# Kernel optimization log

Measured on AMD Instinct MI355X. Metric: run time of the kernel, lower is better.

The kernel has to match this reference:

```python
import jax, jax.numpy as jnp
import numpy as np
from jax import lax

EPS = 1e-5

@jax.custom_vjp
def binarize(x):
    return jnp.sign(x)

def _bin_fwd(x):
    return jnp.sign(x), x

def _bin_bwd(x, g):
    # straight-through estimator: pass grad where |x| <= 1
    return (g * (jnp.abs(x) <= 1.0).astype(g.dtype),)

binarize.defvjp(_bin_fwd, _bin_bwd)


def bconv(x, w, stride=1, pad=0):
    # BinarizeConv2d: sign-binarize both activations and weights, dense conv
    return lax.conv_general_dilated(
        binarize(x), binarize(w),
        window_strides=(stride, stride),
        padding=[(pad, pad), (pad, pad)],
        dimension_numbers=('NCHW', 'OIHW', 'NCHW'))


def bn(x, gamma, beta):
    # training-mode batch norm (grad enabled in torch forward): batch stats over (N,H,W)
    mean = x.mean(axis=(0, 2, 3), keepdims=True)
    var = ((x - mean) ** 2).mean(axis=(0, 2, 3), keepdims=True)
    return gamma * (x - mean) * lax.rsqrt(var + EPS) + beta


def hardtanh(x):
    return jnp.clip(x, -1.0, 1.0)


def setup_inputs() -> dict:
    key = jax.random.key(0)
    ks = jax.random.split(key, 4)
    N, Cin, H, W = 64, 256, 56, 56
    P = 64  # planes; expansion*planes == Cin -> identity shortcut
    return {
        'x':  jax.random.normal(ks[0], (N, Cin, H, W), dtype=jnp.float32),
        'w1': jax.random.normal(ks[1], (P, Cin, 1, 1), dtype=jnp.float32),
        'w2': jax.random.normal(ks[2], (P, P, 3, 3), dtype=jnp.float32),
        'w3': jax.random.normal(ks[3], (Cin, P, 1, 1), dtype=jnp.float32),
        'g1': jnp.ones((1, P, 1, 1), jnp.float32),
        'b1': jnp.zeros((1, P, 1, 1), jnp.float32),
        'g2': jnp.ones((1, P, 1, 1), jnp.float32),
        'b2': jnp.zeros((1, P, 1, 1), jnp.float32),
        'g3': jnp.ones((1, Cin, 1, 1), jnp.float32),
        'b3': jnp.zeros((1, Cin, 1, 1), jnp.float32),
    }


def reference(x, w1, w2, w3, g1, b1, g2, b2, g3, b3):
    out = hardtanh(bn(bconv(x, w1), g1, b1))                 # 1x1 binconv + BN + hardtanh
    out = hardtanh(bn(bconv(out, w2, stride=1, pad=1), g2, b2))  # 3x3 binconv + BN + hardtanh
    out = bn(bconv(out, w3), g3, b3)                          # 1x1 binconv + BN
    out = out + x                                             # identity shortcut
    return hardtanh(out)
```

## Files before the change

kernel.cpp:

```cpp
#include <hip/hip_runtime.h>
#include <stdint.h>
#include <math.h>

typedef unsigned long long u64;
typedef long long ll;

#define H_    56
#define W_    56
#define HW_   3136
#define N_    64
#define C_    256
#define P_    64
#define NPIX_ 200704
#define BN_EPS 1e-5

__global__ __launch_bounds__(256) void pack_weights_k(
    const float* __restrict__ w1, const float* __restrict__ w2,
    const float* __restrict__ w3,
    u64* __restrict__ ws1, u64* __restrict__ wn1,
    u64* __restrict__ ws2, u64* __restrict__ wn2, int* __restrict__ b2,
    u64* __restrict__ ws3, u64* __restrict__ wn3, int* __restrict__ b3) {
  int t = blockIdx.x * 256 + threadIdx.x;
  if (t < 64) {
    int co = t;
    for (int ch = 0; ch < 4; ++ch) {
      u64 s = 0, n = 0;
      for (int j = 0; j < 64; ++j) {
        float v = w1[co * 256 + ch * 64 + j];
        s |= ((u64)(v < 0.f)) << j;
        n |= ((u64)(v != 0.f)) << j;
      }
      ws1[co * 4 + ch] = s; wn1[co * 4 + ch] = n;
    }
  } else if (t < 64 + 576) {
    int idx = t - 64, co = idx / 9, tap = idx % 9;
    u64 s = 0, n = 0;
    for (int ci = 0; ci < 64; ++ci) {
      float v = w2[(co * 64 + ci) * 9 + tap];
      s |= ((u64)(v < 0.f)) << ci;
      n |= ((u64)(v != 0.f)) << ci;
    }
    ws2[idx] = s; wn2[idx] = n; b2[idx] = __popcll(n);
  } else if (t < 64 + 576 + 256) {
    int co = t - 640;
    u64 s = 0, n = 0;
    for (int ci = 0; ci < 64; ++ci) {
      float v = w3[co * 64 + ci];
      s |= ((u64)(v < 0.f)) << ci;
      n |= ((u64)(v != 0.f)) << ci;
    }
    ws3[co] = s; wn3[co] = n; b3[co] = __popcll(n);
  }
}

__device__ inline void bn_thresh(u64 S_, u64 Q_, float g, float b,
                                 int* A, int* X) {
  double S = (double)(ll)S_, Q = (double)(ll)Q_;
  double mean = S / (double)NPIX_;
  double var  = Q / (double)NPIX_ - mean * mean;
  double sc   = (double)g / sqrt(var + BN_EPS);
  double sh   = (double)b - mean * sc;
  if (sc > 0.0) {
    double t = -sh / sc;
    t = fmin(fmax(t, -1.0e8), 1.0e8);
    *A = (int)ceil(t); *X = 0;
  } else if (sc < 0.0) {
    double t = -sh / sc;
    t = fmin(fmax(t, -1.0e8), 1.0e8);
    *A = (int)floor(t) + 1; *X = 1;
  } else {
    *A = (int)0x80000000; *X = (sh < 0.0) ? 1 : 0;
  }
}

__global__ __launch_bounds__(256) void pack_x_k(
    const float* __restrict__ x, u64* __restrict__ xs, u64* __restrict__ xn) {
  int t = blockIdx.x * 256 + threadIdx.x;
  int n = t / 1568;
  int pw = (t - n * 1568) * 2;
  const float* xb = x + (size_t)n * (C_ * HW_) + pw;
  size_t p = (size_t)t * 2;
  for (int q = 0; q < 4; ++q) {
    u64 s0 = 0, s1 = 0, n0 = 0, n1 = 0;
    #pragma unroll 16
    for (int j = 0; j < 64; ++j) {
      float2 v = *(const float2*)(xb + (size_t)(q * 64 + j) * HW_);
      u64 bit = 1ull << j;
      if (v.x <  0.f) s0 |= bit;
      if (v.x != 0.f) n0 |= bit;
      if (v.y <  0.f) s1 |= bit;
      if (v.y != 0.f) n1 |= bit;
    }
    ulonglong2 sv; sv.x = s0; sv.y = s1;
    ulonglong2 nv; nv.x = n0; nv.y = n1;
    *(ulonglong2*)(xs + (size_t)q * NPIX_ + p) = sv;
    *(ulonglong2*)(xn + (size_t)q * NPIX_ + p) = nv;
  }
}

template<int MODE>
__global__ __launch_bounds__(256) void conv1_k(
    const u64* __restrict__ xs, const u64* __restrict__ xn,
    const u64* __restrict__ ws1, const u64* __restrict__ wn1,
    u64* __restrict__ gsum, u64* __restrict__ gsq,
    const float* __restrict__ gamma, const float* __restrict__ beta,
    u64* __restrict__ pout) {
  __shared__ ulonglong2 tile[4][256];
  __shared__ int ssum[64], ssq[64];
  int tid = threadIdx.x, co = tid & 63, wv = tid >> 6;
  int base = blockIdx.x * 256;
  #pragma unroll
  for (int q = 0; q < 4; ++q) {
    ulonglong2 v;
    v.x = xs[(size_t)q * NPIX_ + base + tid];
    v.y = xn[(size_t)q * NPIX_ + base + tid];
    tile[q][tid] = v;
  }
  if (MODE == 0 && tid < 64) { ssum[tid] = 0; ssq[tid] = 0; }
  u64 wS[4], wN[4];
  #pragma unroll
  for (int q = 0; q < 4; ++q) { wS[q] = ws1[co * 4 + q]; wN[q] = wn1[co * 4 + q]; }
  int A = 0, X = 0;
  if (MODE == 1) bn_thresh(gsum[co], gsq[co], gamma[co], beta[co], &A, &X);
  __syncthreads();
  int s = 0, qq = 0;
  u64 mw = 0;
  #pragma unroll 2
  for (int i = 0; i < 64; ++i) {
    int px = wv * 64 + i;
    int acc = 0;
    #pragma unroll
    for (int q = 0; q < 4; ++q) {
      ulonglong2 t2 = tile[q][px];
      u64 v = t2.y & wN[q];
      u64 a = ~(t2.x ^ wS[q]) & v;
      acc += 2 * __popcll(a) - __popcll(v);
    }
    if (MODE == 0) { s += acc; qq += acc * acc; }
    else {
      u64 bal = __ballot((acc < A) ^ X);
      mw = (co == i) ? bal : mw;
    }
  }
  if (MODE == 0) {
    atomicAdd(&ssum[co], s); atomicAdd(&ssq[co], qq);
    __syncthreads();
    if (tid < 64) {
      atomicAdd(&gsum[tid], (u64)(ll)ssum[tid]);
      atomicAdd(&gsq[tid],  (u64)(ll)ssq[tid]);
    }
  } else {
    pout[base + wv * 64 + co] = mw;
  }
}

__device__ inline int c2tap(u64 t, u64 ws, u64 wn) {
  return __popcll(~(t ^ ws) & wn);
}

template<int MODE>
__global__ __launch_bounds__(256) void conv2_k(
    const u64* __restrict__ p1,
    const u64* __restrict__ ws2, const u64* __restrict__ wn2,
    u64* __restrict__ gsum, u64* __restrict__ gsq,
    const float* __restrict__ gamma, const float* __restrict__ beta,
    u64* __restrict__ pout) {
  __shared__ u64 tile[6 * W_];
  __shared__ int ssum[64], ssq[64];
  int tid = threadIdx.x, co = tid & 63, wv = tid >> 6;
  int blk = blockIdx.x;
  int n = blk / 14, t0 = blk - n * 14;
  int h0 = t0 * 4;
  const u64* img = p1 + (size_t)n * HW_;
  for (int j = tid; j < 6 * W_; j += 256) {
    int gh = h0 - 1 + j / W_;
    int gw = j - (j / W_) * W_;
    tile[j] = (gh >= 0 && gh < H_) ? img[gh * W_ + gw] : 0ull;
  }
  if (MODE == 0 && tid < 64) { ssum[tid] = 0; ssq[tid] = 0; }
  u64 wS[9], wN[9]; int wB[9], Bs = 0;
  #pragma unroll
  for (int k = 0; k < 9; ++k) {
    wS[k] = ws2[co * 9 + k]; wN[k] = wn2[co * 9 + k];
    wB[k] = __popcll(wN[k]); Bs += wB[k];
  }
  int A = 0, X = 0;
  if (MODE == 1) bn_thresh(gsum[co], gsq[co], gamma[co], beta[co], &A, &X);
  __syncthreads();
  int h = h0 + wv;
  const u64* rA = tile + wv * W_;
  const u64* rB = rA + W_;
  const u64* rC = rB + W_;
  int vA = (h > 0), vC = (h < H_ - 1);
  int s = 0, qq = 0;
  u64 mw = 0;
  if (vA & vC) {
    {
      int P = c2tap(rA[0], wS[1], wN[1]) + c2tap(rA[1], wS[2], wN[2])
            + c2tap(rB[0], wS[4], wN[4]) + c2tap(rB[1], wS[5], wN[5])
            + c2tap(rC[0], wS[7], wN[7]) + c2tap(rC[1], wS[8], wN[8]);
      int acc = 2 * P - (wB[1] + wB[2] + wB[4] + wB[5] + wB[7] + wB[8]);
      if (MODE == 0) { s += acc; qq += acc * acc; }
      else { u64 bal = __ballot((acc < A) ^ X); mw = (co == 0) ? bal : mw; }
    }
    #pragma unroll 2
    for (int w = 1; w < W_ - 1; ++w) {
      int P = c2tap(rA[w-1], wS[0], wN[0]) + c2tap(rA[w], wS[1], wN[1]) + c2tap(rA[w+1], wS[2], wN[2])
            + c2tap(rB[w-1], wS[3], wN[3]) + c2tap(rB[w], wS[4], wN[4]) + c2tap(rB[w+1], wS[5], wN[5])
            + c2tap(rC[w-1], wS[6], wN[6]) + c2tap(rC[w], wS[7], wN[7]) + c2tap(rC[w+1], wS[8], wN[8]);
      int acc = 2 * P - Bs;
      if (MODE == 0) { s += acc; qq += acc * acc; }
      else { u64 bal = __ballot((acc < A) ^ X); mw = (co == w) ? bal : mw; }
    }
    {
      int P = c2tap(rA[W_-2], wS[0], wN[0]) + c2tap(rA[W_-1], wS[1], wN[1])
            + c2tap(rB[W_-2], wS[3], wN[3]) + c2tap(rB[W_-1], wS[4], wN[4])
            + c2tap(rC[W_-2], wS[6], wN[6]) + c2tap(rC[W_-1], wS[7], wN[7]);
      int acc = 2 * P - (wB[0] + wB[1] + wB[3] + wB[4] + wB[6] + wB[7]);
      if (MODE == 0) { s += acc; qq += acc * acc; }
      else { u64 bal = __ballot((acc < A) ^ X); mw = (co == W_ - 1) ? bal : mw; }
    }
  } else {
    for (int w = 0; w < W_; ++w) {
      int wm = w > 0, wp = w < W_ - 1;
      int P = 0, B = 0;
      if (vA) {
        if (wm) { P += c2tap(rA[w-1], wS[0], wN[0]); B += wB[0]; }
        P += c2tap(rA[w], wS[1], wN[1]); B += wB[1];
        if (wp) { P += c2tap(rA[w+1], wS[2], wN[2]); B += wB[2]; }
      }
      if (wm) { P += c2tap(rB[w-1], wS[3], wN[3]); B += wB[3]; }
      P += c2tap(rB[w], wS[4], wN[4]); B += wB[4];
      if (wp) { P += c2tap(rB[w+1], wS[5], wN[5]); B += wB[5]; }
      if (vC) {
        if (wm) { P += c2tap(rC[w-1], wS[6], wN[6]); B += wB[6]; }
        P += c2tap(rC[w], wS[7], wN[7]); B += wB[7];
        if (wp) { P += c2tap(rC[w+1], wS[8], wN[8]); B += wB[8]; }
      }
      int acc = 2 * P - B;
      if (MODE == 0) { s += acc; qq += acc * acc; }
      else { u64 bal = __ballot((acc < A) ^ X); mw = (co == w) ? bal : mw; }
    }
  }
  if (MODE == 0) {
    atomicAdd(&ssum[co], s); atomicAdd(&ssq[co], qq);
    __syncthreads();
    if (tid < 64) {
      atomicAdd(&gsum[tid], (u64)(ll)ssum[tid]);
      atomicAdd(&gsq[tid],  (u64)(ll)ssq[tid]);
    }
  } else {
    if (co < W_) pout[(size_t)n * HW_ + h * W_ + co] = mw;
  }
}

__global__ __launch_bounds__(256) void conv3_stats_k(
    const u64* __restrict__ p2,
    const u64* __restrict__ ws3, const u64* __restrict__ wn3,
    const int* __restrict__ b3,
    u64* __restrict__ gsum, u64* __restrict__ gsq) {
  __shared__ u64 tile[512];
  int t = threadIdx.x;
  int base = blockIdx.x * 512;
  *(ulonglong2*)&tile[t * 2] = *(const ulonglong2*)&p2[base + t * 2];
  u64 s3 = ws3[t], n3 = wn3[t];
  int bb = b3[t];
  __syncthreads();
  int s = 0, q = 0;
  #pragma unroll 4
  for (int i = 0; i < 512; ++i) {
    int yv = 2 * __popcll(~(tile[i] ^ s3) & n3) - bb;
    s += yv; q += yv * yv;
  }
  atomicAdd(&gsum[t], (u64)(ll)s);
  atomicAdd(&gsq[t],  (u64)(ll)q);
}

__global__ __launch_bounds__(256) void final_k(
    const float* __restrict__ x, const u64* __restrict__ p2,
    const u64* __restrict__ ws3, const u64* __restrict__ wn3,
    const int* __restrict__ b3,
    const u64* __restrict__ gsum, const u64* __restrict__ gsq,
    const float* __restrict__ gamma, const float* __restrict__ beta,
    float* __restrict__ out) {
  __shared__ float fsc[2], fsh[2];
  size_t base = (size_t)blockIdx.x * 1024;
  size_t r0 = base / HW_;
  if (threadIdx.x < 2) {
    int c = (int)((r0 + threadIdx.x) % C_);
    double S = (double)(ll)gsum[c], Q = (double)(ll)gsq[c];
    double mean = S / (double)NPIX_;
    double var  = Q / (double)NPIX_ - mean * mean;
    double inv  = 1.0 / sqrt(var + BN_EPS);
    double sc   = (double)gamma[c] * inv;
    fsc[threadIdx.x] = (float)sc;
    fsh[threadIdx.x] = (float)((double)beta[c] - mean * sc);
  }
  __syncthreads();

  size_t idx = base + (size_t)threadIdx.x * 4;
  size_t lin = idx / HW_;
  int rr = (int)(lin - r0);
  int co = (int)(lin % C_);
  int nn = (int)(lin / C_);
  int hw = (int)(idx % HW_);
  int pb = nn * HW_ + hw;
  u64 s3 = ws3[co], n3 = wn3[co];
  int bb = b3[co];
  float sc = fsc[rr], sh = fsh[rr];
  float4 xv = *(const float4*)(x + idx);
  float4 ov;
  int y0 = 2 * __popcll(~(p2[pb + 0] ^ s3) & n3) - bb;
  int y1 = 2 * __popcll(~(p2[pb + 1] ^ s3) & n3) - bb;
  int y2 = 2 * __popcll(~(p2[pb + 2] ^ s3) & n3) - bb;
  int y3 = 2 * __popcll(~(p2[pb + 3] ^ s3) & n3) - bb;
  ov.x = fminf(fmaxf(sc * (float)y0 + sh + xv.x, -1.f), 1.f);
  ov.y = fminf(fmaxf(sc * (float)y1 + sh + xv.y, -1.f), 1.f);
  ov.z = fminf(fmaxf(sc * (float)y2 + sh + xv.z, -1.f), 1.f);
  ov.w = fminf(fmaxf(sc * (float)y3 + sh + xv.w, -1.f), 1.f);
  *(float4*)(out + idx) = ov;
}

extern "C" void kernel_launch(void* const* d_in, const int* in_sizes, int n_in,
                              void* d_out, int out_size, void* d_ws, size_t ws_size,
                              hipStream_t stream) {
  const float* x  = (const float*)d_in[0];
  const float* w1 = (const float*)d_in[1];
  const float* w2 = (const float*)d_in[2];
  const float* w3 = (const float*)d_in[3];
  const float* g1 = (const float*)d_in[4];
  const float* b1 = (const float*)d_in[5];
  const float* g2 = (const float*)d_in[6];
  const float* b2 = (const float*)d_in[7];
  const float* g3 = (const float*)d_in[8];
  const float* b3 = (const float*)d_in[9];
  float* out = (float*)d_out;

  char* base = (char*)d_ws;
  size_t off = 0;
  auto alloc = [&](size_t bytes) -> char* {
    char* p = base + off;
    off = (off + bytes + 255) & ~(size_t)255;
    return p;
  };
  u64* xs   = (u64*)alloc((size_t)NPIX_ * 4 * 8);
  u64* xnz  = (u64*)alloc((size_t)NPIX_ * 4 * 8);
  u64* p1   = (u64*)alloc((size_t)NPIX_ * 8);
  u64* p2   = (u64*)alloc((size_t)NPIX_ * 8);
  u64* ws1  = (u64*)alloc(256 * 8);
  u64* wn1  = (u64*)alloc(256 * 8);
  u64* ws2  = (u64*)alloc(576 * 8);
  u64* wn2  = (u64*)alloc(576 * 8);
  int* bb2  = (int*)alloc(576 * 4);
  u64* ws3  = (u64*)alloc(256 * 8);
  u64* wn3  = (u64*)alloc(256 * 8);
  int* bb3  = (int*)alloc(256 * 4);
  char* stats = alloc(768 * 8);
  u64* sum1 = (u64*)stats;          u64* sq1 = sum1 + 64;
  u64* sum2 = sq1 + 64;             u64* sq2 = sum2 + 64;
  u64* sum3 = sq2 + 64;             u64* sq3 = sum3 + 256;
  (void)ws_size; (void)n_in; (void)in_sizes; (void)out_size;

  hipMemsetAsync(stats, 0, 768 * 8, stream);

  pack_weights_k<<<4, 256, 0, stream>>>(w1, w2, w3, ws1, wn1, ws2, wn2, bb2,
                                        ws3, wn3, bb3);

  pack_x_k<<<392, 256, 0, stream>>>(x, xs, xnz);

  conv1_k<0><<<784, 256, 0, stream>>>(xs, xnz, ws1, wn1, sum1, sq1,
                                      g1, b1, (u64*)nullptr);
  conv1_k<1><<<784, 256, 0, stream>>>(xs, xnz, ws1, wn1, sum1, sq1,
                                      g1, b1, p1);

  conv2_k<0><<<896, 256, 0, stream>>>(p1, ws2, wn2, sum2, sq2,
                                      g2, b2, (u64*)nullptr);
  conv2_k<1><<<896, 256, 0, stream>>>(p1, ws2, wn2, sum2, sq2,
                                      g2, b2, p2);

  conv3_stats_k<<<392, 256, 0, stream>>>(p2, ws3, wn3, bb3, sum3, sq3);

  final_k<<<50176, 256, 0, stream>>>(x, p2, ws3, wn3, bb3, sum3, sq3, g3, b3,
                                     out);
}
```

Before: 589.7 us.

## Split x packing and conv1 across more blocks; precompute BN3 scale table

pack_x now assigns one 64-channel group per block, which quadruples the grid and gives more loads in flight for the strided channel reads. conv1 handles 128 pixels per block instead of 256, doubling its grid, though half the lanes of each wave now sit idle in the ballot-and-store path. The BN3 scale/shift computation moves out of every final_k block into a single small kernel that writes a per-channel table. This removes the double-precision math and the __syncthreads from final_k at the cost of one extra launch.

```diff
diff --git a/kernel.cpp b/kernel.cpp
--- a/kernel.cpp
+++ b/kernel.cpp
@@ -75,27 +75,26 @@
 
 __global__ __launch_bounds__(256) void pack_x_k(
     const float* __restrict__ x, u64* __restrict__ xs, u64* __restrict__ xn) {
-  int t = blockIdx.x * 256 + threadIdx.x;
+  int t = (blockIdx.x >> 2) * 256 + threadIdx.x;
+  int q = blockIdx.x & 3;
   int n = t / 1568;
   int pw = (t - n * 1568) * 2;
-  const float* xb = x + (size_t)n * (C_ * HW_) + pw;
+  const float* xb = x + (size_t)n * (C_ * HW_) + (size_t)(q * 64) * HW_ + pw;
+  u64 s0 = 0, s1 = 0, n0 = 0, n1 = 0;
+  #pragma unroll 16
+  for (int j = 0; j < 64; ++j) {
+    float2 v = *(const float2*)(xb + (size_t)j * HW_);
+    u64 bit = 1ull << j;
+    if (v.x <  0.f) s0 |= bit;
+    if (v.x != 0.f) n0 |= bit;
+    if (v.y <  0.f) s1 |= bit;
+    if (v.y != 0.f) n1 |= bit;
+  }
   size_t p = (size_t)t * 2;
-  for (int q = 0; q < 4; ++q) {
-    u64 s0 = 0, s1 = 0, n0 = 0, n1 = 0;
-    #pragma unroll 16
-    for (int j = 0; j < 64; ++j) {
-      float2 v = *(const float2*)(xb + (size_t)(q * 64 + j) * HW_);
-      u64 bit = 1ull << j;
-      if (v.x <  0.f) s0 |= bit;
-      if (v.x != 0.f) n0 |= bit;
-      if (v.y <  0.f) s1 |= bit;
-      if (v.y != 0.f) n1 |= bit;
-    }
-    ulonglong2 sv; sv.x = s0; sv.y = s1;
-    ulonglong2 nv; nv.x = n0; nv.y = n1;
-    *(ulonglong2*)(xs + (size_t)q * NPIX_ + p) = sv;
-    *(ulonglong2*)(xn + (size_t)q * NPIX_ + p) = nv;
-  }
+  ulonglong2 sv; sv.x = s0; sv.y = s1;
+  ulonglong2 nv; nv.x = n0; nv.y = n1;
+  *(ulonglong2*)(xs + (size_t)q * NPIX_ + p) = sv;
+  *(ulonglong2*)(xn + (size_t)q * NPIX_ + p) = nv;
 }
 
 template<int MODE>
@@ -105,16 +104,17 @@
     u64* __restrict__ gsum, u64* __restrict__ gsq,
     const float* __restrict__ gamma, const float* __restrict__ beta,
     u64* __restrict__ pout) {
-  __shared__ ulonglong2 tile[4][256];
+  __shared__ ulonglong2 tile[4][128];
   __shared__ int ssum[64], ssq[64];
   int tid = threadIdx.x, co = tid & 63, wv = tid >> 6;
-  int base = blockIdx.x * 256;
+  int base = blockIdx.x * 128;
   #pragma unroll
-  for (int q = 0; q < 4; ++q) {
+  for (int e = tid; e < 512; e += 256) {
+    int q = e >> 7, px = e & 127;
     ulonglong2 v;
-    v.x = xs[(size_t)q * NPIX_ + base + tid];
-    v.y = xn[(size_t)q * NPIX_ + base + tid];
-    tile[q][tid] = v;
+    v.x = xs[(size_t)q * NPIX_ + base + px];
+    v.y = xn[(size_t)q * NPIX_ + base + px];
+    tile[q][px] = v;
   }
   if (MODE == 0 && tid < 64) { ssum[tid] = 0; ssq[tid] = 0; }
   u64 wS[4], wN[4];
@@ -126,8 +126,8 @@
   int s = 0, qq = 0;
   u64 mw = 0;
   #pragma unroll 2
-  for (int i = 0; i < 64; ++i) {
-    int px = wv * 64 + i;
+  for (int i = 0; i < 32; ++i) {
+    int px = wv * 32 + i;
     int acc = 0;
     #pragma unroll
     for (int q = 0; q < 4; ++q) {
@@ -150,7 +150,7 @@
       atomicAdd(&gsq[tid],  (u64)(ll)ssq[tid]);
     }
   } else {
-    pout[base + wv * 64 + co] = mw;
+    if (co < 32) pout[base + wv * 32 + co] = mw;
   }
 }
 
@@ -276,38 +276,37 @@
   atomicAdd(&gsq[t],  (u64)(ll)q);
 }
 
+__global__ __launch_bounds__(256) void thresh3_k(
+    const u64* __restrict__ gsum, const u64* __restrict__ gsq,
+    const float* __restrict__ gamma, const float* __restrict__ beta,
+    float2* __restrict__ tab) {
+  int c = threadIdx.x;
+  double S = (double)(ll)gsum[c], Q = (double)(ll)gsq[c];
+  double mean = S / (double)NPIX_;
+  double var  = Q / (double)NPIX_ - mean * mean;
+  double inv  = 1.0 / sqrt(var + BN_EPS);
+  double sc   = (double)gamma[c] * inv;
+  float2 r;
+  r.x = (float)sc;
+  r.y = (float)((double)beta[c] - mean * sc);
+  tab[c] = r;
+}
+
 __global__ __launch_bounds__(256) void final_k(
     const float* __restrict__ x, const u64* __restrict__ p2,
     const u64* __restrict__ ws3, const u64* __restrict__ wn3,
-    const int* __restrict__ b3,
-    const u64* __restrict__ gsum, const u64* __restrict__ gsq,
-    const float* __restrict__ gamma, const float* __restrict__ beta,
+    const int* __restrict__ b3, const float2* __restrict__ tab,
     float* __restrict__ out) {
-  __shared__ float fsc[2], fsh[2];
-  size_t base = (size_t)blockIdx.x * 1024;
-  size_t r0 = base / HW_;
-  if (threadIdx.x < 2) {
-    int c = (int)((r0 + threadIdx.x) % C_);
-    double S = (double)(ll)gsum[c], Q = (double)(ll)gsq[c];
-    double mean = S / (double)NPIX_;
-    double var  = Q / (double)NPIX_ - mean * mean;
-    double inv  = 1.0 / sqrt(var + BN_EPS);
-    double sc   = (double)gamma[c] * inv;
-    fsc[threadIdx.x] = (float)sc;
-    fsh[threadIdx.x] = (float)((double)beta[c] - mean * sc);
-  }
-  __syncthreads();
-
-  size_t idx = base + (size_t)threadIdx.x * 4;
+  size_t idx = ((size_t)blockIdx.x * 256 + threadIdx.x) * 4;
   size_t lin = idx / HW_;
-  int rr = (int)(lin - r0);
   int co = (int)(lin % C_);
   int nn = (int)(lin / C_);
   int hw = (int)(idx % HW_);
   int pb = nn * HW_ + hw;
   u64 s3 = ws3[co], n3 = wn3[co];
   int bb = b3[co];
-  float sc = fsc[rr], sh = fsh[rr];
+  float2 th = tab[co];
+  float sc = th.x, sh = th.y;
   float4 xv = *(const float4*)(x + idx);
   float4 ov;
   int y0 = 2 * __popcll(~(p2[pb + 0] ^ s3) & n3) - bb;
@@ -355,6 +354,7 @@
   u64* ws3  = (u64*)alloc(256 * 8);
   u64* wn3  = (u64*)alloc(256 * 8);
   int* bb3  = (int*)alloc(256 * 4);
+  float2* tab3 = (float2*)alloc(256 * 8);
   char* stats = alloc(768 * 8);
   u64* sum1 = (u64*)stats;          u64* sq1 = sum1 + 64;
   u64* sum2 = sq1 + 64;             u64* sq2 = sum2 + 64;
@@ -366,12 +366,12 @@
   pack_weights_k<<<4, 256, 0, stream>>>(w1, w2, w3, ws1, wn1, ws2, wn2, bb2,
                                         ws3, wn3, bb3);
 
-  pack_x_k<<<392, 256, 0, stream>>>(x, xs, xnz);
-
-  conv1_k<0><<<784, 256, 0, stream>>>(xs, xnz, ws1, wn1, sum1, sq1,
-                                      g1, b1, (u64*)nullptr);
-  conv1_k<1><<<784, 256, 0, stream>>>(xs, xnz, ws1, wn1, sum1, sq1,
-                                      g1, b1, p1);
+  pack_x_k<<<1568, 256, 0, stream>>>(x, xs, xnz);
+
+  conv1_k<0><<<1568, 256, 0, stream>>>(xs, xnz, ws1, wn1, sum1, sq1,
+                                       g1, b1, (u64*)nullptr);
+  conv1_k<1><<<1568, 256, 0, stream>>>(xs, xnz, ws1, wn1, sum1, sq1,
+                                       g1, b1, p1);
 
   conv2_k<0><<<896, 256, 0, stream>>>(p1, ws2, wn2, sum2, sq2,
                                       g2, b2, (u64*)nullptr);
@@ -379,7 +379,7 @@
                                       g2, b2, p2);
 
   conv3_stats_k<<<392, 256, 0, stream>>>(p2, ws3, wn3, bb3, sum3, sq3);
-
-  final_k<<<50176, 256, 0, stream>>>(x, p2, ws3, wn3, bb3, sum3, sq3, g3, b3,
-                                     out);
-}
+  thresh3_k<<<1, 256, 0, stream>>>(sum3, sq3, g3, b3, tab3);
+
+  final_k<<<50176, 256, 0, stream>>>(x, p2, ws3, wn3, bb3, tab3, out);
+}
```

After: 574.9 us. 2.5% less time.
